# Optimization experiments

Measured on AMD Instinct MI355X. Metric: run time of the kernel, lower is better.

## Reference

```python
import jax, jax.numpy as jnp
import numpy as np

C = 64
G = 4          # group_number
K = 3          # kernel_size
R = 4          # reduction_ratio -> bottleneck C//R = 16
BN_EPS = 1e-3  # keras BatchNormalization default epsilon


def setup_inputs() -> dict:
    key = jax.random.key(0)
    ks = jax.random.split(key, 8)
    B, H, W = 8, 192, 192
    cr = C // R
    x = jax.random.normal(ks[0], (B, H, W, C), dtype=jnp.float32)
    # kernel_gen: Conv2D 1x1 (C -> C//R), BN, ReLU, Conv2D 1x1 (C//R -> K*K*G)
    w1 = jax.random.normal(ks[1], (C, cr), dtype=jnp.float32) * (1.0 / np.sqrt(C))
    b1 = jnp.zeros((cr,), dtype=jnp.float32)
    gamma = 1.0 + 0.1 * jax.random.normal(ks[2], (cr,), dtype=jnp.float32)
    beta = 0.1 * jax.random.normal(ks[3], (cr,), dtype=jnp.float32)
    mean = 0.1 * jax.random.normal(ks[4], (cr,), dtype=jnp.float32)
    var = jax.random.uniform(ks[5], (cr,), dtype=jnp.float32, minval=0.5, maxval=1.5)
    w2 = jax.random.normal(ks[6], (cr, K * K * G), dtype=jnp.float32) * (1.0 / np.sqrt(cr))
    b2 = jnp.zeros((K * K * G,), dtype=jnp.float32)
    return {"x": x, "w1": w1, "b1": b1, "gamma": gamma, "beta": beta,
            "mean": mean, "var": var, "w2": w2, "b2": b2}


def reference(x, w1, b1, gamma, beta, mean, var, w2, b2):
    B, H, W, Cc = x.shape
    # --- kernel generation (stride=1 -> identity pooling) ---
    t = jnp.einsum('bhwc,cd->bhwd', x, w1) + b1                 # [B,H,W,C//R]
    t = (t - mean) * jax.lax.rsqrt(var + BN_EPS) * gamma + beta  # BN (inference)
    t = jax.nn.relu(t)
    kern = jnp.einsum('bhwd,de->bhwe', t, w2) + b2               # [B,H,W,K*K*G]
    kern = kern.reshape(B, H, W, K * K, 1, G)
    # --- unfold: tf.image.extract_patches SAME, stride 1, patch order (ki,kj,C) ---
    pad = K // 2
    xp = jnp.pad(x, ((0, 0), (pad, pad), (pad, pad), (0, 0)))
    patches = jnp.stack(
        [xp[:, i:i + H, j:j + W, :] for i in range(K) for j in range(K)],
        axis=3)                                                  # [B,H,W,K*K,C]
    unfolded = patches.reshape(B, H, W, K * K, Cc // G, G)
    # --- per-pixel multiply-reduce over patch axis ---
    out = jnp.sum(kern * unfolded, axis=3)                       # [B,H,W,C//G,G]
    return out.reshape(B, H, W, Cc)
```

## Files before the change

kernel.cpp:

```cpp
#include <hip/hip_runtime.h>


#define B_   8
#define H_   192
#define W_   192
#define CR_  16
#define TH_  8
#define TW_  16
#define TILES_X (W_/TW_)
#define TILES_PER_IMG (TILES_X*(H_/TH_))
#define NBLK (B_*TILES_PER_IMG)
#define NPIX (TH_*TW_)
#define XSTRIDE 17

constexpr float BN_EPS = 1e-3f;

__device__ __forceinline__ float4 mask4(float4 k, bool v) {
    k.x = v ? k.x : 0.f;
    k.y = v ? k.y : 0.f;
    k.z = v ? k.z : 0.f;
    k.w = v ? k.w : 0.f;
    return k;
}

__device__ __forceinline__ void fma4(float4& a, const float4 k, const float4 x) {
    a.x = fmaf(k.x, x.x, a.x);
    a.y = fmaf(k.y, x.y, a.y);
    a.z = fmaf(k.z, x.z, a.z);
    a.w = fmaf(k.w, x.w, a.w);
}

#define LROWS(S, R)                                                         \
    do {                                                                    \
        int rr_ = (R);                                                      \
        if (!INTERIOR) {                                                    \
            if ((unsigned)rr_ < (unsigned)H_) rv |= (1 << (S));             \
            else                              rv &= ~(1 << (S));            \
            rr_ = rr_ < 0 ? 0 : (rr_ >= H_ ? H_ - 1 : rr_);                 \
        }                                                                   \
        const int rb_ = rr_ * (W_ * 16);                                    \
        rgA[S][0] = x4[rb_ + coA[0]];                                       \
        rgA[S][1] = x4[rb_ + coA[1]];                                       \
        rgA[S][2] = x4[rb_ + coA[2]];                                       \
        rgB[S][0] = x4[rb_ + coB[0]];                                       \
        rgB[S][1] = x4[rb_ + coB[1]];                                       \
        rgB[S][2] = x4[rb_ + coB[2]];                                       \
    } while (0)

#define COMP(I)                                                             \
    do {                                                                    \
        const float4* kqA_ = &s_kern[((I) * TW_ + wslot) * 9];              \
        const float4* kqB_ = &s_kern[((I) * TW_ + wslot + 8) * 9];          \
        float4 aA_ = make_float4(0.f, 0.f, 0.f, 0.f);                       \
        float4 aB_ = make_float4(0.f, 0.f, 0.f, 0.f);                       \
        _Pragma("unroll")                                                   \
        for (int ti_ = 0; ti_ < 3; ++ti_) {                                 \
            const int s_ = ((I) + ti_) & 3;                                 \
            _Pragma("unroll")                                               \
            for (int tj_ = 0; tj_ < 3; ++tj_) {                             \
                float4 kA_ = kqA_[ti_ * 3 + tj_];                           \
                float4 kB_ = kqB_[ti_ * 3 + tj_];                           \
                if (!INTERIOR) {                                            \
                    kA_ = mask4(kA_, (((rv >> s_) & (cmA >> tj_)) & 1));    \
                    kB_ = mask4(kB_, (((rv >> s_) & (cmB >> tj_)) & 1));    \
                }                                                           \
                fma4(aA_, kA_, rgA[s_][tj_]);                               \
                fma4(aB_, kB_, rgB[s_][tj_]);                               \
            }                                                               \
        }                                                                   \
        const int ob_ = (th0 + (I)) * (W_ * 16);                            \
        o4[ob_ + (wA << 4) + c4i] = aA_;                                    \
        o4[ob_ + (wB << 4) + c4i] = aB_;                                    \
    } while (0)

#define SFENCE __builtin_amdgcn_sched_barrier(0)

template <bool INTERIOR>
__device__ __forceinline__ void phase_b(const float4* __restrict__ x4,
                                        float4* __restrict__ o4,
                                        const float4* __restrict__ s_kern,
                                        int th0, int tw0, int tid)
{
    const int wslot = tid >> 4;
    const int c4i   = tid & 15;
    const int wA = tw0 + wslot;
    const int wB = tw0 + wslot + 8;

    int coA[3], coB[3];
    int cmA = 7, cmB = 7;
    #pragma unroll
    for (int tj = 0; tj < 3; ++tj) {
        int wa = wA + tj - 1;
        int wb = wB + tj - 1;
        if (!INTERIOR) {
            if ((unsigned)wa >= (unsigned)W_) cmA &= ~(1 << tj);
            if ((unsigned)wb >= (unsigned)W_) cmB &= ~(1 << tj);
            wa = wa < 0 ? 0 : (wa >= W_ ? W_ - 1 : wa);
            wb = wb < 0 ? 0 : (wb >= W_ ? W_ - 1 : wb);
        }
        coA[tj] = (wa << 4) + c4i;
        coB[tj] = (wb << 4) + c4i;
    }

    float4 rgA[4][3], rgB[4][3];
    int rv = 0xF;

    LROWS(0, th0 - 1);
    LROWS(1, th0 + 0);
    LROWS(2, th0 + 1);
    LROWS(3, th0 + 2);
    SFENCE;
    COMP(0); LROWS(0, th0 + 3);
    SFENCE;
    COMP(1); LROWS(1, th0 + 4);
    SFENCE;
    COMP(2); LROWS(2, th0 + 5);
    SFENCE;
    COMP(3); LROWS(3, th0 + 6);
    SFENCE;
    COMP(4); LROWS(0, th0 + 7);
    SFENCE;
    COMP(5); LROWS(1, th0 + 8);
    SFENCE;
    COMP(6);
    COMP(7);
}

#undef LROWS
#undef COMP

__global__ __launch_bounds__(128, 2)
void invol_fused(const float* __restrict__ x,
                 const float* __restrict__ w1,
                 const float* __restrict__ b1,
                 const float* __restrict__ gamma,
                 const float* __restrict__ beta,
                 const float* __restrict__ mean,
                 const float* __restrict__ var,
                 const float* __restrict__ w2,
                 const float* __restrict__ b2,
                 float* __restrict__ out)
{
    __shared__ float4 smem[NPIX * XSTRIDE];

    const int bid = blockIdx.x;
    const int img = bid & 7;
    const int tin = bid >> 3;
    const int th0 = (tin / TILES_X) * TH_;
    const int tw0 = (tin % TILES_X) * TW_;
    const int tid = threadIdx.x;

    const float4* x4 = reinterpret_cast<const float4*>(x) +
                       (size_t)img * (H_ * W_ * 16);
    float4* o4 = reinterpret_cast<float4*>(out) +
                 (size_t)img * (H_ * W_ * 16);

    {
        const int rowbase = th0 * (W_ * 16) + (tw0 << 4);
        #pragma unroll
        for (int i = 0; i < 16; ++i) {
            const int lin = i * 128 + tid;
            const int r   = lin >> 8;
            const int c   = lin & 255;
            const float4 v = x4[rowbase + r * (W_ * 16) + c];
            smem[(r * 16 + (c >> 4)) * XSTRIDE + (c & 15)] = v;
        }
    }
    __syncthreads();

    float ke[36];
    {
        float td[CR_];
        #pragma unroll
        for (int d = 0; d < CR_; ++d) td[d] = 0.f;

        #pragma unroll
        for (int c4 = 0; c4 < 16; ++c4) {
            const float4 xv = smem[tid * XSTRIDE + c4];
            const float xs[4] = {xv.x, xv.y, xv.z, xv.w};
            #pragma unroll
            for (int k = 0; k < 4; ++k) {
                const float* wr = w1 + (c4 * 4 + k) * CR_;
                #pragma unroll
                for (int d = 0; d < CR_; ++d)
                    td[d] = fmaf(xs[k], wr[d], td[d]);
            }
        }

        __syncthreads();

        #pragma unroll
        for (int d = 0; d < CR_; ++d) {
            const float a = gamma[d] * rsqrtf(var[d] + BN_EPS);
            const float c = (b1[d] - mean[d]) * a + beta[d];
            td[d] = fmaxf(fmaf(td[d], a, c), 0.f);
        }

        #pragma unroll
        for (int e = 0; e < 36; ++e) ke[e] = b2[e];
        #pragma unroll
        for (int d = 0; d < CR_; ++d) {
            const float t = td[d];
            const float* wr = w2 + d * 36;
            #pragma unroll
            for (int e = 0; e < 36; ++e)
                ke[e] = fmaf(t, wr[e], ke[e]);
        }
    }

    {
        float4* skq = &smem[tid * 9];
        #pragma unroll
        for (int t9 = 0; t9 < 9; ++t9)
            skq[t9] = make_float4(ke[t9 * 4 + 0], ke[t9 * 4 + 1],
                                  ke[t9 * 4 + 2], ke[t9 * 4 + 3]);
    }

    __syncthreads();

    const float4* s_kern = smem;
    const bool interior = (th0 > 0) && (th0 + TH_ < H_) &&
                          (tw0 > 0) && (tw0 + TW_ < W_);
    if (interior)
        phase_b<true >(x4, o4, s_kern, th0, tw0, tid);
    else
        phase_b<false>(x4, o4, s_kern, th0, tw0, tid);
}

extern "C" void kernel_launch(void* const* d_in, const int* in_sizes, int n_in,
                              void* d_out, int out_size, void* d_ws, size_t ws_size,
                              hipStream_t stream) {
    const float* x     = (const float*)d_in[0];
    const float* w1    = (const float*)d_in[1];
    const float* b1    = (const float*)d_in[2];
    const float* gamma = (const float*)d_in[3];
    const float* beta  = (const float*)d_in[4];
    const float* mean  = (const float*)d_in[5];
    const float* var   = (const float*)d_in[6];
    const float* w2    = (const float*)d_in[7];
    const float* b2    = (const float*)d_in[8];
    float* out = (float*)d_out;

    invol_fused<<<dim3(NBLK), dim3(128), 0, stream>>>(
        x, w1, b1, gamma, beta, mean, var, w2, b2, out);
}
```

Baseline: 207.8 us.

## Give each wavefront its own LDS region with XOR swizzle, drop block barriers

Each 64-lane wavefront now stages its own four rows of the input tile in a private LDS region, using an XOR swizzle in place of the stride-17 padding, and writes its generated kernels into that same region. This removes two of the three block-wide barriers in the kernel-generation phase, keeping one barrier before phase B reads kernels written by the other wave. It also shrinks LDS from 17*128 to 2048 float4s, which could raise occupancy. The risk is that correctness now depends on intra-wave ordering of LDS writes and reads, with no barrier between them.

```diff
diff --git a/kernel.cpp b/kernel.cpp
--- a/kernel.cpp
+++ b/kernel.cpp
@@ -11,7 +11,7 @@
 #define TILES_PER_IMG (TILES_X*(H_/TH_))
 #define NBLK (B_*TILES_PER_IMG)
 #define NPIX (TH_*TW_)
-#define XSTRIDE 17
+#define WREG 1024
 
 constexpr float BN_EPS = 1e-3f;
 
@@ -49,8 +49,10 @@
 
 #define COMP(I)                                                             \
     do {                                                                    \
-        const float4* kqA_ = &s_kern[((I) * TW_ + wslot) * 9];              \
-        const float4* kqB_ = &s_kern[((I) * TW_ + wslot + 8) * 9];          \
+        const float4* kqA_ = &s_kern[((I) >> 2) * WREG +                    \
+                                     (((I) & 3) * TW_ + wslot) * 9];        \
+        const float4* kqB_ = &s_kern[((I) >> 2) * WREG +                    \
+                                     (((I) & 3) * TW_ + wslot + 8) * 9];    \
         float4 aA_ = make_float4(0.f, 0.f, 0.f, 0.f);                       \
         float4 aB_ = make_float4(0.f, 0.f, 0.f, 0.f);                       \
         _Pragma("unroll")                                                   \
@@ -109,6 +111,9 @@
     LROWS(1, th0 + 0);
     LROWS(2, th0 + 1);
     LROWS(3, th0 + 2);
+
+    __syncthreads();
+
     SFENCE;
     COMP(0); LROWS(0, th0 + 3);
     SFENCE;
@@ -141,7 +146,7 @@
                  const float* __restrict__ b2,
                  float* __restrict__ out)
 {
-    __shared__ float4 smem[NPIX * XSTRIDE];
+    __shared__ float4 smem[2 * WREG];
 
     const int bid = blockIdx.x;
     const int img = bid & 7;
@@ -149,6 +154,8 @@
     const int th0 = (tin / TILES_X) * TH_;
     const int tw0 = (tin % TILES_X) * TW_;
     const int tid = threadIdx.x;
+    const int wv  = tid >> 6;
+    const int ln  = tid & 63;
 
     const float4* x4 = reinterpret_cast<const float4*>(x) +
                        (size_t)img * (H_ * W_ * 16);
@@ -156,27 +163,28 @@
                  (size_t)img * (H_ * W_ * 16);
 
     {
-        const int rowbase = th0 * (W_ * 16) + (tw0 << 4);
+        float4* sx = &smem[wv * WREG];
+        const int rowbase = (th0 + 4 * wv) * (W_ * 16) + (tw0 << 4);
         #pragma unroll
         for (int i = 0; i < 16; ++i) {
-            const int lin = i * 128 + tid;
-            const int r   = lin >> 8;
-            const int c   = lin & 255;
-            const float4 v = x4[rowbase + r * (W_ * 16) + c];
-            smem[(r * 16 + (c >> 4)) * XSTRIDE + (c & 15)] = v;
-        }
-    }
-    __syncthreads();
+            const float4 v = x4[rowbase + (i >> 2) * (W_ * 16) +
+                                (i & 3) * 64 + ln];
+            const int p = 4 * i + (ln >> 4);
+            sx[p * 16 + ((ln & 15) ^ (p & 7))] = v;
+        }
+    }
 
     float ke[36];
     {
+        const float4* sx = &smem[wv * WREG + ln * 16];
+        const int sw = ln & 7;
         float td[CR_];
         #pragma unroll
         for (int d = 0; d < CR_; ++d) td[d] = 0.f;
 
         #pragma unroll
         for (int c4 = 0; c4 < 16; ++c4) {
-            const float4 xv = smem[tid * XSTRIDE + c4];
+            const float4 xv = sx[c4 ^ sw];
             const float xs[4] = {xv.x, xv.y, xv.z, xv.w};
             #pragma unroll
             for (int k = 0; k < 4; ++k) {
@@ -187,8 +195,6 @@
             }
         }
 
-        __syncthreads();
-
         #pragma unroll
         for (int d = 0; d < CR_; ++d) {
             const float a = gamma[d] * rsqrtf(var[d] + BN_EPS);
@@ -209,22 +215,19 @@
     }
 
     {
-        float4* skq = &smem[tid * 9];
+        float4* skq = &smem[wv * WREG + ln * 9];
         #pragma unroll
         for (int t9 = 0; t9 < 9; ++t9)
             skq[t9] = make_float4(ke[t9 * 4 + 0], ke[t9 * 4 + 1],
                                   ke[t9 * 4 + 2], ke[t9 * 4 + 3]);
     }
 
-    __syncthreads();
-
-    const float4* s_kern = smem;
     const bool interior = (th0 > 0) && (th0 + TH_ < H_) &&
                           (tw0 > 0) && (tw0 + TW_ < W_);
     if (interior)
-        phase_b<true >(x4, o4, s_kern, th0, tw0, tid);
+        phase_b<true >(x4, o4, smem, th0, tw0, tid);
     else
-        phase_b<false>(x4, o4, s_kern, th0, tw0, tid);
+        phase_b<false>(x4, o4, smem, th0, tw0, tid);
 }
 
 extern "C" void kernel_launch(void* const* d_in, const int* in_sizes, int n_in,
```

Measured after the change: 178.9 us. -13.9%, faster.
